# Kernel optimization log

Hardware: AMD Instinct MI355X
Metric: run time of the kernel (lower is better)

## Reference

```python
import jax, jax.numpy as jnp
import numpy as np

N, E, IN, HID, H, C, NL, OUT = 50000, 500000, 384, 128, 8, 16, 3, 16
NEG_SLOPE = 0.2

def setup_inputs() -> dict:
    key = jax.random.key(0)
    ks = jax.random.split(key, 16)
    s = 0.1
    return {
        "x": jax.random.normal(ks[0], (N, IN), jnp.float32),
        "edge_index": jax.random.randint(ks[1], (2, E), 0, N, jnp.int32),
        "proj_w": jax.random.normal(ks[2], (IN, HID), jnp.float32) * s,
        "proj_b": jax.random.normal(ks[3], (HID,), jnp.float32) * s,
        "lin_w": jax.random.normal(ks[4], (NL, HID, HID), jnp.float32) * s,
        "att_src": jax.random.normal(ks[5], (NL, H, C), jnp.float32) * s,
        "att_dst": jax.random.normal(ks[6], (NL, H, C), jnp.float32) * s,
        "gat_b": jax.random.normal(ks[7], (NL, HID), jnp.float32) * s,
        "ln_g": jnp.ones((NL, HID), jnp.float32),
        "ln_b": jnp.zeros((NL, HID), jnp.float32),
        "cls_w1": jax.random.normal(ks[8], (HID, HID // 2), jnp.float32) * s,
        "cls_b1": jax.random.normal(ks[9], (HID // 2,), jnp.float32) * s,
        "cls_w2": jax.random.normal(ks[10], (HID // 2, OUT), jnp.float32) * s,
        "cls_b2": jax.random.normal(ks[11], (OUT,), jnp.float32) * s,
    }

def _layernorm(h, g, b, eps=1e-5):
    mu = jnp.mean(h, axis=-1, keepdims=True)
    var = jnp.var(h, axis=-1, keepdims=True)
    return (h - mu) * jax.lax.rsqrt(var + eps) * g + b

def _gat_layer(h, src, dst, w, a_src, a_dst, bias):
    # h: [N, HID]; per-head transform -> [N, H, C]
    xh = (h @ w).reshape(N, H, C)
    al_s = jnp.einsum('nhc,hc->nh', xh, a_src)   # [N, H]
    al_d = jnp.einsum('nhc,hc->nh', xh, a_dst)
    e = jax.nn.leaky_relu(al_s[src] + al_d[dst], NEG_SLOPE)  # [E+N, H]
    # segment softmax over incoming edges of each dst node
    m = jax.ops.segment_max(e, dst, num_segments=N)
    e = jnp.exp(e - m[dst])
    denom = jax.ops.segment_sum(e, dst, num_segments=N)
    alpha = e / (denom[dst] + 1e-16)
    msg = xh[src] * alpha[:, :, None]            # [E+N, H, C]
    out = jax.ops.segment_sum(msg, dst, num_segments=N)
    return out.reshape(N, H * C) + bias

def reference(x, edge_index, proj_w, proj_b, lin_w, att_src, att_dst, gat_b,
              ln_g, ln_b, cls_w1, cls_b1, cls_w2, cls_b2):
    loops = jnp.arange(N, dtype=edge_index.dtype)  # PyG GATConv adds self-loops
    src = jnp.concatenate([edge_index[0], loops])
    dst = jnp.concatenate([edge_index[1], loops])
    h = jax.nn.relu(x @ proj_w + proj_b)
    for l in range(NL):
        h_res = h
        h = _gat_layer(h, src, dst, lin_w[l], att_src[l], att_dst[l], gat_b[l])
        h = h + h_res
        h = jax.nn.relu(_layernorm(h, ln_g[l], ln_b[l]))
    logits = jax.nn.relu(h @ cls_w1 + cls_b1) @ cls_w2 + cls_b2
    return jax.nn.log_softmax(logits, axis=1)
```

## Files before the change

kernel.cpp:

```cpp
#include <hip/hip_runtime.h>
#include <hip/hip_bf16.h>
#include <math.h>

#define NN 50000
#define EE 500000
#define DIN 384
#define HIDD 128
#define NHEAD 8
#define OUTD 16

typedef __attribute__((ext_vector_type(8))) __bf16 bf16x8;
typedef __attribute__((ext_vector_type(4))) float f32x4;

__device__ __forceinline__ ushort f2bf(float f) {
  union { float f; unsigned u; } v; v.f = f;
  unsigned r = v.u + 0x7fffu + ((v.u >> 16) & 1u);
  return (ushort)(r >> 16);
}
__device__ __forceinline__ float bflo(unsigned w) {
  union { unsigned u; float f; } v; v.u = w << 16; return v.f;
}
__device__ __forceinline__ float bfhi(unsigned w) {
  union { unsigned u; float f; } v; v.u = w & 0xffff0000u; return v.f;
}

__global__ void zero_ints(int* p, int n) {
  int i = blockIdx.x * blockDim.x + threadIdx.x;
  if (i < n) p[i] = 0;
}

__global__ void hist_kernel(const int* __restrict__ dst, int* __restrict__ counts, int e) {
  int i = blockIdx.x * blockDim.x + threadIdx.x;
  if (i < e) atomicAdd(&counts[dst[i]], 1);
}

#define SCAN_BS 256
#define SCAN_NBLK ((NN + SCAN_BS - 1) / SCAN_BS)

__global__ __launch_bounds__(256) void partial_sums(const int* __restrict__ counts,
                                                    int* __restrict__ bsum, int n) {
  __shared__ int red[256];
  int i = blockIdx.x * 256 + threadIdx.x;
  red[threadIdx.x] = (i < n) ? counts[i] : 0;
  __syncthreads();
  #pragma unroll
  for (int off = 128; off; off >>= 1) {
    if (threadIdx.x < off) red[threadIdx.x] += red[threadIdx.x + off];
    __syncthreads();
  }
  if (threadIdx.x == 0) bsum[blockIdx.x] = red[0];
}

__global__ __launch_bounds__(256) void scan_bsums(const int* __restrict__ bsum,
                                                  int* __restrict__ boff, int nb) {
  __shared__ int buf[256];
  int t = threadIdx.x;
  int v = (t < nb) ? bsum[t] : 0;
  buf[t] = v;
  __syncthreads();
  #pragma unroll
  for (int off = 1; off < 256; off <<= 1) {
    int u = (t >= off) ? buf[t - off] : 0;
    __syncthreads();
    buf[t] += u;
    __syncthreads();
  }
  if (t < nb) boff[t] = buf[t] - v;
}

__global__ __launch_bounds__(256) void final_scan(const int* __restrict__ counts,
                                                  const int* __restrict__ boff,
                                                  int* __restrict__ rowptr,
                                                  int* __restrict__ woff, int n) {
  __shared__ int buf[256];
  int i = blockIdx.x * 256 + threadIdx.x;
  int t = threadIdx.x;
  int v = (i < n) ? counts[i] : 0;
  buf[t] = v;
  __syncthreads();
  #pragma unroll
  for (int off = 1; off < 256; off <<= 1) {
    int u = (t >= off) ? buf[t - off] : 0;
    __syncthreads();
    buf[t] += u;
    __syncthreads();
  }
  int excl = boff[blockIdx.x] + buf[t] - v;
  if (i < n) { rowptr[i] = excl; woff[i] = excl; }
  if (i == n - 1) rowptr[n] = excl + v;
}

__global__ void scatter_kernel(const int* __restrict__ src, const int* __restrict__ dst,
                               int* __restrict__ woff, int* __restrict__ col, int e) {
  int i = blockIdx.x * blockDim.x + threadIdx.x;
  if (i < e) {
    int p = atomicAdd(&woff[dst[i]], 1);
    col[p] = src[i];
  }
}

__global__ void prep_weights(const float* __restrict__ proj_w,
                             const float* __restrict__ lin_w,
                             const float* __restrict__ cls_w1,
                             const float* __restrict__ cls_w2,
                             ushort* __restrict__ wt) {
  int i = blockIdx.x * blockDim.x + threadIdx.x;
  if (i < 49152) {
    int k = i >> 7, n = i & 127;
    wt[n * 384 + k] = f2bf(proj_w[i]);
  } else if (i < 98304) {
    int j = i - 49152;
    int l = j >> 14, rem = j & 16383;
    int k = rem >> 7, n = rem & 127;
    wt[49152 + l * 16384 + n * 128 + k] = f2bf(lin_w[j]);
  } else if (i < 106496) {
    int j = i - 98304;
    int n = j >> 7, k = j & 127;
    wt[98304 + n * 128 + k] = f2bf(cls_w1[k * 64 + n]);
  } else if (i < 107520) {
    int j = i - 106496;
    int n = j >> 6, k = j & 63;
    wt[106496 + n * 64 + k] = f2bf(cls_w2[k * 16 + n]);
  }
}

#define LDS_STRIDE 72
template<typename AT, bool RELU_BIAS>
__global__ __launch_bounds__(256) void mfma_gemm64(const AT* __restrict__ A,
                                                   const ushort* __restrict__ Bt,
                                                   const float* __restrict__ bias,
                                                   ushort* __restrict__ C, int M, int K) {
  __shared__ ushort sA[64 * LDS_STRIDE];
  __shared__ ushort sB[128 * LDS_STRIDE];
  const int tid = threadIdx.x;
  const int wave = tid >> 6, lane = tid & 63;
  const int q = lane >> 4, lm = lane & 15;
  const int wr = wave >> 1, wc = wave & 1;
  const int m0 = blockIdx.x * 64;

  f32x4 acc[2][4];
  #pragma unroll
  for (int i = 0; i < 2; i++)
    #pragma unroll
    for (int j = 0; j < 4; j++) acc[i][j] = {0.f, 0.f, 0.f, 0.f};

  for (int k0 = 0; k0 < K; k0 += 64) {
    __syncthreads();
    if constexpr (sizeof(AT) == 4) {
      #pragma unroll
      for (int p = 0; p < 4; ++p) {
        int idx = p * 256 + tid;
        int r = idx >> 4;
        int c = (idx & 15) << 2;
        int row = min(m0 + r, M - 1);
        float4 v = *(const float4*)((const float*)A + (size_t)row * K + k0 + c);
        ushort4 u;
        u.x = f2bf(v.x); u.y = f2bf(v.y); u.z = f2bf(v.z); u.w = f2bf(v.w);
        *(ushort4*)&sA[r * LDS_STRIDE + c] = u;
      }
    } else {
      #pragma unroll
      for (int p = 0; p < 2; ++p) {
        int idx = p * 256 + tid;
        int r = idx >> 3;
        int c = (idx & 7) << 3;
        int row = min(m0 + r, M - 1);
        *(bf16x8*)&sA[r * LDS_STRIDE + c] =
            *(const bf16x8*)((const ushort*)A + (size_t)row * K + k0 + c);
      }
    }
    #pragma unroll
    for (int p = 0; p < 4; ++p) {
      int idx = p * 256 + tid;
      int r = idx >> 3;
      int c = (idx & 7) << 3;
      *(bf16x8*)&sB[r * LDS_STRIDE + c] = *(const bf16x8*)(Bt + (size_t)r * K + k0 + c);
    }
    __syncthreads();
    #pragma unroll
    for (int ks = 0; ks < 2; ++ks) {
      bf16x8 af[2], bfv[4];
      #pragma unroll
      for (int t = 0; t < 2; ++t)
        af[t] = *(const bf16x8*)&sA[(wr * 32 + t * 16 + lm) * LDS_STRIDE + ks * 32 + q * 8];
      #pragma unroll
      for (int t = 0; t < 4; ++t)
        bfv[t] = *(const bf16x8*)&sB[(wc * 64 + t * 16 + lm) * LDS_STRIDE + ks * 32 + q * 8];
      #pragma unroll
      for (int i = 0; i < 2; ++i)
        #pragma unroll
        for (int j = 0; j < 4; ++j)
          acc[i][j] = __builtin_amdgcn_mfma_f32_16x16x32_bf16(af[i], bfv[j], acc[i][j], 0, 0, 0);
    }
  }
  #pragma unroll
  for (int i = 0; i < 2; ++i) {
    #pragma unroll
    for (int r = 0; r < 4; ++r) {
      int row = m0 + wr * 32 + i * 16 + q * 4 + r;
      if (row < M) {
        #pragma unroll
        for (int j = 0; j < 4; ++j) {
          int colc = wc * 64 + j * 16 + lm;
          float v = acc[i][j][r];
          if (RELU_BIAS) { v += bias[colc]; v = fmaxf(v, 0.f); }
          C[(size_t)row * 128 + colc] = f2bf(v);
        }
      }
    }
  }
}

__global__ void att_logits_kernel(const ushort* __restrict__ xh,
                                  const float* __restrict__ att_s,
                                  const float* __restrict__ att_d,
                                  float* __restrict__ al_s, float* __restrict__ al_d, int n) {
  int t = blockIdx.x * blockDim.x + threadIdx.x;
  if (t >= n * NHEAD) return;
  int head = t & 7;
  const unsigned* xw = (const unsigned*)(xh + (size_t)t * 16);
  const float* as = att_s + head * 16;
  const float* ad = att_d + head * 16;
  float ss = 0.f, dd = 0.f;
  #pragma unroll
  for (int i = 0; i < 8; ++i) {
    unsigned w = xw[i];
    float x0 = bflo(w), x1 = bfhi(w);
    ss = fmaf(x0, as[i * 2], fmaf(x1, as[i * 2 + 1], ss));
    dd = fmaf(x0, ad[i * 2], fmaf(x1, ad[i * 2 + 1], dd));
  }
  al_s[t] = ss;
  al_d[t] = dd;
}

__global__ __launch_bounds__(256) void gat_aggregate(
    const ushort* __restrict__ xh, const float* __restrict__ al_s,
    const float* __restrict__ al_d, const int* __restrict__ rowptr,
    const int* __restrict__ col, const ushort* __restrict__ h_res,
    const float* __restrict__ gb, const float* __restrict__ lng,
    const float* __restrict__ lnb, ushort* __restrict__ h_out, int n) {
  const int lane = threadIdx.x & 63;
  const int node = (blockIdx.x * blockDim.x + threadIdx.x) >> 6;
  if (node >= n) return;
  const int e8 = lane >> 3;
  const int hh = lane & 7;
  const int head = lane >> 3;
  const unsigned* xw_base = (const unsigned*)xh;

  const int start = rowptr[node], end = rowptr[node + 1];
  const int T = end - start + 1;
  const float ald_c = al_d[node * 8 + hh];

  float m = -INFINITY, denom = 0.f, acc0 = 0.f, acc1 = 0.f;

  for (int c = 0; c < T; c += 8) {
    int it = c + e8;
    bool valid = it < T;
    int idx = start + it;
    int s = (valid && idx < end) ? col[idx] : node;
    float e = al_s[s * 8 + hh] + ald_c;
    e = (e > 0.f) ? e : 0.2f * e;
    if (!valid) e = -INFINITY;
    float cm = e;
    cm = fmaxf(cm, __shfl_xor(cm, 8));
    cm = fmaxf(cm, __shfl_xor(cm, 16));
    cm = fmaxf(cm, __shfl_xor(cm, 32));
    float newm = fmaxf(m, __shfl(cm, head));
    float newm_c = __shfl(newm, hh * 8);
    float p_lane = __expf(e - newm_c);
    float scale = __expf(m - newm);
    m = newm;
    unsigned xg[8];
    int sj[8];
    #pragma unroll
    for (int j = 0; j < 8; ++j) sj[j] = __shfl(s, j * 8);
    #pragma unroll
    for (int j = 0; j < 8; ++j) xg[j] = xw_base[(size_t)sj[j] * 64 + lane];
    denom *= scale; acc0 *= scale; acc1 *= scale;
    #pragma unroll
    for (int j = 0; j < 8; ++j) {
      float pj = __shfl(p_lane, j * 8 + head);
      denom += pj;
      acc0 = fmaf(pj, bflo(xg[j]), acc0);
      acc1 = fmaf(pj, bfhi(xg[j]), acc1);
    }
  }

  float inv = 1.f / denom;
  int c0 = lane * 2, c1 = c0 + 1;
  unsigned ur = ((const unsigned*)h_res)[(size_t)node * 64 + lane];
  float v0 = acc0 * inv + gb[c0] + bflo(ur);
  float v1 = acc1 * inv + gb[c1] + bfhi(ur);
  float sum = v0 + v1;
  #pragma unroll
  for (int off = 32; off; off >>= 1) sum += __shfl_xor(sum, off);
  float mean = sum * (1.f / 128.f);
  float d0 = v0 - mean, d1 = v1 - mean;
  float sq = d0 * d0 + d1 * d1;
  #pragma unroll
  for (int off = 32; off; off >>= 1) sq += __shfl_xor(sq, off);
  float rstd = rsqrtf(sq * (1.f / 128.f) + 1e-5f);
  float o0 = fmaxf(d0 * rstd * lng[c0] + lnb[c0], 0.f);
  float o1 = fmaxf(d1 * rstd * lng[c1] + lnb[c1], 0.f);
  ((unsigned*)h_out)[(size_t)node * 64 + lane] =
      (unsigned)f2bf(o0) | ((unsigned)f2bf(o1) << 16);
}

#define CSTR 136
#define HSTR 72
__global__ __launch_bounds__(256) void classifier_mfma(
    const ushort* __restrict__ h, const ushort* __restrict__ w1t,
    const float* __restrict__ b1, const ushort* __restrict__ w2t,
    const float* __restrict__ b2, float* __restrict__ out, int n) {
  __shared__ ushort sA[128 * CSTR];
  __shared__ ushort sB[64 * CSTR];
  __shared__ ushort sHid[128 * HSTR];
  const int tid = threadIdx.x;
  const int wave = tid >> 6, lane = tid & 63;
  const int q = lane >> 4, lm = lane & 15;
  const int wr = wave >> 1, wc = wave & 1;
  const int m0 = blockIdx.x * 128;

  #pragma unroll
  for (int p = 0; p < 8; ++p) {
    int idx = p * 256 + tid;
    int r = idx >> 4;
    int c = (idx & 15) << 3;
    int row = min(m0 + r, n - 1);
    *(bf16x8*)&sA[r * CSTR + c] = *(const bf16x8*)(h + (size_t)row * 128 + c);
  }
  #pragma unroll
  for (int p = 0; p < 4; ++p) {
    int idx = p * 256 + tid;
    int r = idx >> 4;
    int c = (idx & 15) << 3;
    *(bf16x8*)&sB[r * CSTR + c] = *(const bf16x8*)(w1t + r * 128 + c);
  }
  __syncthreads();

  f32x4 acc[4][2];
  #pragma unroll
  for (int i = 0; i < 4; ++i)
    #pragma unroll
    for (int j = 0; j < 2; ++j) acc[i][j] = {0.f, 0.f, 0.f, 0.f};
  #pragma unroll
  for (int ks = 0; ks < 4; ++ks) {
    bf16x8 af[4], bfv[2];
    #pragma unroll
    for (int t = 0; t < 4; ++t)
      af[t] = *(const bf16x8*)&sA[(wr * 64 + t * 16 + lm) * CSTR + ks * 32 + q * 8];
    #pragma unroll
    for (int j = 0; j < 2; ++j)
      bfv[j] = *(const bf16x8*)&sB[(wc * 32 + j * 16 + lm) * CSTR + ks * 32 + q * 8];
    #pragma unroll
    for (int i = 0; i < 4; ++i)
      #pragma unroll
      for (int j = 0; j < 2; ++j)
        acc[i][j] = __builtin_amdgcn_mfma_f32_16x16x32_bf16(af[i], bfv[j], acc[i][j], 0, 0, 0);
  }
  #pragma unroll
  for (int i = 0; i < 4; ++i) {
    #pragma unroll
    for (int j = 0; j < 2; ++j) {
      int colc = wc * 32 + j * 16 + lm;
      float bb = b1[colc];
      #pragma unroll
      for (int r = 0; r < 4; ++r) {
        int row = wr * 64 + i * 16 + q * 4 + r;
        float v = fmaxf(acc[i][j][r] + bb, 0.f);
        sHid[row * HSTR + colc] = f2bf(v);
      }
    }
  }
  __syncthreads();

  f32x4 acc2[2] = {{0.f, 0.f, 0.f, 0.f}, {0.f, 0.f, 0.f, 0.f}};
  #pragma unroll
  for (int ks = 0; ks < 2; ++ks) {
    bf16x8 b2f = *(const bf16x8*)(w2t + lm * 64 + ks * 32 + q * 8);
    #pragma unroll
    for (int t = 0; t < 2; ++t) {
      bf16x8 a2 = *(const bf16x8*)&sHid[(wave * 32 + t * 16 + lm) * HSTR + ks * 32 + q * 8];
      acc2[t] = __builtin_amdgcn_mfma_f32_16x16x32_bf16(a2, b2f, acc2[t], 0, 0, 0);
    }
  }
  float bb2 = b2[lm];
  #pragma unroll
  for (int t = 0; t < 2; ++t) {
    #pragma unroll
    for (int r = 0; r < 4; ++r) {
      int row = m0 + wave * 32 + t * 16 + q * 4 + r;
      float lg = acc2[t][r] + bb2;
      float mx = lg;
      #pragma unroll
      for (int off = 8; off; off >>= 1) mx = fmaxf(mx, __shfl_xor(mx, off, 16));
      float se = __expf(lg - mx);
      #pragma unroll
      for (int off = 8; off; off >>= 1) se += __shfl_xor(se, off, 16);
      if (row < n) out[(size_t)row * 16 + lm] = lg - mx - __logf(se);
    }
  }
}

extern "C" void kernel_launch(void* const* d_in, const int* in_sizes, int n_in,
                              void* d_out, int out_size, void* d_ws, size_t ws_size,
                              hipStream_t stream) {
  const float* x       = (const float*)d_in[0];
  const int*   ei      = (const int*)d_in[1];
  const float* proj_w  = (const float*)d_in[2];
  const float* proj_b  = (const float*)d_in[3];
  const float* lin_w   = (const float*)d_in[4];
  const float* att_src = (const float*)d_in[5];
  const float* att_dst = (const float*)d_in[6];
  const float* gat_b   = (const float*)d_in[7];
  const float* ln_g    = (const float*)d_in[8];
  const float* ln_b    = (const float*)d_in[9];
  const float* cls_w1  = (const float*)d_in[10];
  const float* cls_b1  = (const float*)d_in[11];
  const float* cls_w2  = (const float*)d_in[12];
  const float* cls_b2  = (const float*)d_in[13];
  float* outp = (float*)d_out;

  const int N = NN, E = EE;
  ushort* wt   = (ushort*)d_ws;
  ushort* h0   = wt + 108544;
  ushort* h1   = h0 + (size_t)N * 128;
  ushort* xh_u = h1 + (size_t)N * 128;
  float* als   = (float*)(xh_u + (size_t)N * 128);
  float* ald   = als + (size_t)N * NHEAD;
  int* counts  = (int*)(ald + (size_t)N * NHEAD);
  int* rowptr  = counts + N;
  int* woff    = rowptr + N + 1;
  int* col     = woff + N;
  int* bsum    = col + E;
  int* boff    = bsum + SCAN_NBLK;

  const int* e_src = ei;
  const int* e_dst = ei + E;

  prep_weights<<<(107520 + 255) / 256, 256, 0, stream>>>(proj_w, lin_w, cls_w1, cls_w2, wt);

  zero_ints<<<(N + 255) / 256, 256, 0, stream>>>(counts, N);
  hist_kernel<<<(E + 255) / 256, 256, 0, stream>>>(e_dst, counts, E);
  partial_sums<<<SCAN_NBLK, 256, 0, stream>>>(counts, bsum, N);
  scan_bsums<<<1, 256, 0, stream>>>(bsum, boff, SCAN_NBLK);
  final_scan<<<SCAN_NBLK, 256, 0, stream>>>(counts, boff, rowptr, woff, N);
  scatter_kernel<<<(E + 255) / 256, 256, 0, stream>>>(e_src, e_dst, woff, col, E);

  const int gblocks = (N + 63) / 64;
  mfma_gemm64<float, true><<<gblocks, 256, 0, stream>>>(x, wt, proj_b, h0, N, DIN);

  ushort* hc = h0;
  ushort* hn = h1;
  for (int l = 0; l < 3; ++l) {
    mfma_gemm64<ushort, false><<<gblocks, 256, 0, stream>>>(
        hc, wt + 49152 + l * 16384, nullptr, xh_u, N, 128);
    att_logits_kernel<<<(N * NHEAD + 255) / 256, 256, 0, stream>>>(
        xh_u, att_src + l * 128, att_dst + l * 128, als, ald, N);
    gat_aggregate<<<(N + 3) / 4, 256, 0, stream>>>(
        xh_u, als, ald, rowptr, col, hc, gat_b + l * 128, ln_g + l * 128,
        ln_b + l * 128, hn, N);
    ushort* t = hc; hc = hn; hn = t;
  }
  classifier_mfma<<<(N + 127) / 128, 256, 0, stream>>>(
      hc, wt + 98304, cls_b1, wt + 106496, cls_b2, outp, N);
}
```

Measured before the change: 380.2 us.

## Fuse attention logits into GAT GEMM epilogue and widen aggregate gather batch

Removes the separate attention-logit kernel by computing the per-head src/dst dot products in the GEMM epilogue, reducing across the 16 columns of each head with lane shuffles on the fp32 accumulators. This saves a kernel launch and a re-read of xh per layer. The aggregate kernel now processes 16 edges per iteration, issuing two batches of neighbour-row gathers before the softmax math to keep more loads in flight. In exchange, logits now come from fp32 accumulators rather than bf16-rounded values, the epilogue carries many extra shuffles, and the wider loop adds per-edge branches and register pressure.

```diff
diff --git a/kernel.cpp b/kernel.cpp
--- a/kernel.cpp
+++ b/kernel.cpp
@@ -125,11 +125,16 @@
 }
 
 #define LDS_STRIDE 72
-template<typename AT, bool RELU_BIAS>
+template<typename AT, bool RELU_BIAS, bool ATT>
 __global__ __launch_bounds__(256) void mfma_gemm64(const AT* __restrict__ A,
                                                    const ushort* __restrict__ Bt,
                                                    const float* __restrict__ bias,
-                                                   ushort* __restrict__ C, int M, int K) {
+                                                   ushort* __restrict__ C,
+                                                   const float* __restrict__ att_s,
+                                                   const float* __restrict__ att_d,
+                                                   float* __restrict__ al_s,
+                                                   float* __restrict__ al_d,
+                                                   int M, int K) {
   __shared__ ushort sA[64 * LDS_STRIDE];
   __shared__ ushort sB[128 * LDS_STRIDE];
   const int tid = threadIdx.x;
@@ -191,6 +196,14 @@
         #pragma unroll
         for (int j = 0; j < 4; ++j)
           acc[i][j] = __builtin_amdgcn_mfma_f32_16x16x32_bf16(af[i], bfv[j], acc[i][j], 0, 0, 0);
+    }
+  }
+  float asw[4], adw[4];
+  if constexpr (ATT) {
+    #pragma unroll
+    for (int j = 0; j < 4; ++j) {
+      asw[j] = att_s[(wc * 4 + j) * 16 + lm];
+      adw[j] = att_d[(wc * 4 + j) * 16 + lm];
     }
   }
   #pragma unroll
@@ -209,28 +222,31 @@
       }
     }
   }
-}
-
-__global__ void att_logits_kernel(const ushort* __restrict__ xh,
-                                  const float* __restrict__ att_s,
-                                  const float* __restrict__ att_d,
-                                  float* __restrict__ al_s, float* __restrict__ al_d, int n) {
-  int t = blockIdx.x * blockDim.x + threadIdx.x;
-  if (t >= n * NHEAD) return;
-  int head = t & 7;
-  const unsigned* xw = (const unsigned*)(xh + (size_t)t * 16);
-  const float* as = att_s + head * 16;
-  const float* ad = att_d + head * 16;
-  float ss = 0.f, dd = 0.f;
-  #pragma unroll
-  for (int i = 0; i < 8; ++i) {
-    unsigned w = xw[i];
-    float x0 = bflo(w), x1 = bfhi(w);
-    ss = fmaf(x0, as[i * 2], fmaf(x1, as[i * 2 + 1], ss));
-    dd = fmaf(x0, ad[i * 2], fmaf(x1, ad[i * 2 + 1], dd));
-  }
-  al_s[t] = ss;
-  al_d[t] = dd;
+  if constexpr (ATT) {
+    #pragma unroll
+    for (int i = 0; i < 2; ++i) {
+      #pragma unroll
+      for (int j = 0; j < 4; ++j) {
+        #pragma unroll
+        for (int r = 0; r < 4; ++r) {
+          float ss = acc[i][j][r] * asw[j];
+          float dd = acc[i][j][r] * adw[j];
+          #pragma unroll
+          for (int off = 1; off < 16; off <<= 1) {
+            ss += __shfl_xor(ss, off);
+            dd += __shfl_xor(dd, off);
+          }
+          if (lm == 0) {
+            int row = m0 + wr * 32 + i * 16 + q * 4 + r;
+            if (row < M) {
+              al_s[row * 8 + wc * 4 + j] = ss;
+              al_d[row * 8 + wc * 4 + j] = dd;
+            }
+          }
+        }
+      }
+    }
+  }
 }
 
 __global__ __launch_bounds__(256) void gat_aggregate(
@@ -253,37 +269,61 @@
 
   float m = -INFINITY, denom = 0.f, acc0 = 0.f, acc1 = 0.f;
 
-  for (int c = 0; c < T; c += 8) {
-    int it = c + e8;
-    bool valid = it < T;
-    int idx = start + it;
-    int s = (valid && idx < end) ? col[idx] : node;
-    float e = al_s[s * 8 + hh] + ald_c;
-    e = (e > 0.f) ? e : 0.2f * e;
-    if (!valid) e = -INFINITY;
-    float cm = e;
+  for (int c = 0; c < T; c += 16) {
+    int it0 = c + e8, it1 = c + 8 + e8;
+    int idx0 = start + it0, idx1 = start + it1;
+    int s0 = (it0 < T && idx0 < end) ? col[idx0] : node;
+    int s1 = (it1 < T && idx1 < end) ? col[idx1] : node;
+
+    unsigned xg0[8], xg1[8];
+    #pragma unroll
+    for (int j = 0; j < 8; ++j)
+      if (c + j < T) {
+        int sj = __shfl(s0, j * 8);
+        xg0[j] = xw_base[(size_t)sj * 64 + lane];
+      }
+    #pragma unroll
+    for (int j = 0; j < 8; ++j)
+      if (c + 8 + j < T) {
+        int sj = __shfl(s1, j * 8);
+        xg1[j] = xw_base[(size_t)sj * 64 + lane];
+      }
+
+    float e0 = al_s[s0 * 8 + hh] + ald_c;
+    e0 = (e0 > 0.f) ? e0 : 0.2f * e0;
+    if (it0 >= T) e0 = -INFINITY;
+    float e1 = al_s[s1 * 8 + hh] + ald_c;
+    e1 = (e1 > 0.f) ? e1 : 0.2f * e1;
+    if (it1 >= T) e1 = -INFINITY;
+
+    float cm = fmaxf(e0, e1);
     cm = fmaxf(cm, __shfl_xor(cm, 8));
     cm = fmaxf(cm, __shfl_xor(cm, 16));
     cm = fmaxf(cm, __shfl_xor(cm, 32));
     float newm = fmaxf(m, __shfl(cm, head));
     float newm_c = __shfl(newm, hh * 8);
-    float p_lane = __expf(e - newm_c);
+    float p0 = __expf(e0 - newm_c);
+    float p1 = __expf(e1 - newm_c);
     float scale = __expf(m - newm);
     m = newm;
-    unsigned xg[8];
-    int sj[8];
-    #pragma unroll
-    for (int j = 0; j < 8; ++j) sj[j] = __shfl(s, j * 8);
-    #pragma unroll
-    for (int j = 0; j < 8; ++j) xg[j] = xw_base[(size_t)sj[j] * 64 + lane];
+
     denom *= scale; acc0 *= scale; acc1 *= scale;
     #pragma unroll
-    for (int j = 0; j < 8; ++j) {
-      float pj = __shfl(p_lane, j * 8 + head);
-      denom += pj;
-      acc0 = fmaf(pj, bflo(xg[j]), acc0);
-      acc1 = fmaf(pj, bfhi(xg[j]), acc1);
-    }
+    for (int j = 0; j < 8; ++j)
+      if (c + j < T) {
+        float pj = __shfl(p0, j * 8 + head);
+        denom += pj;
+        acc0 = fmaf(pj, bflo(xg0[j]), acc0);
+        acc1 = fmaf(pj, bfhi(xg0[j]), acc1);
+      }
+    #pragma unroll
+    for (int j = 0; j < 8; ++j)
+      if (c + 8 + j < T) {
+        float pj = __shfl(p1, j * 8 + head);
+        denom += pj;
+        acc0 = fmaf(pj, bflo(xg1[j]), acc0);
+        acc1 = fmaf(pj, bfhi(xg1[j]), acc1);
+      }
   }
 
   float inv = 1.f / denom;
@@ -448,15 +488,15 @@
   scatter_kernel<<<(E + 255) / 256, 256, 0, stream>>>(e_src, e_dst, woff, col, E);
 
   const int gblocks = (N + 63) / 64;
-  mfma_gemm64<float, true><<<gblocks, 256, 0, stream>>>(x, wt, proj_b, h0, N, DIN);
+  mfma_gemm64<float, true, false><<<gblocks, 256, 0, stream>>>(
+      x, wt, proj_b, h0, nullptr, nullptr, nullptr, nullptr, N, DIN);
 
   ushort* hc = h0;
   ushort* hn = h1;
   for (int l = 0; l < 3; ++l) {
-    mfma_gemm64<ushort, false><<<gblocks, 256, 0, stream>>>(
-        hc, wt + 49152 + l * 16384, nullptr, xh_u, N, 128);
-    att_logits_kernel<<<(N * NHEAD + 255) / 256, 256, 0, stream>>>(
-        xh_u, att_src + l * 128, att_dst + l * 128, als, ald, N);
+    mfma_gemm64<ushort, false, true><<<gblocks, 256, 0, stream>>>(
+        hc, wt + 49152 + l * 16384, nullptr, xh_u,
+        att_src + l * 128, att_dst + l * 128, als, ald, N, 128);
     gat_aggregate<<<(N + 3) / 4, 256, 0, stream>>>(
         xh_u, als, ald, rowptr, col, hc, gat_b + l * 128, ln_g + l * 128,
         ln_b + l * 128, hn, N);
```

Result: slower. 402.5 us (+5.9%).

## Fuse attention logits into GEMM epilogue and shrink GEMM tile to 32 rows

Applied to the files above, without the earlier changes.

Computes the per-head attention logits in the layer GEMM epilogue using shuffle reductions over the fp32 accumulators, which removes the separate att_logits kernel and its re-read of xh. The GEMM tile drops from 64 to 32 rows, giving twice as many blocks for occupancy, and K becomes a template constant. The trade-off is that each block now re-reads the full B matrix for half as many rows, and the logits come from fp32 accumulators instead of bf16-rounded values.

```diff
diff --git a/kernel.cpp b/kernel.cpp
--- a/kernel.cpp
+++ b/kernel.cpp
@@ -125,83 +125,93 @@
 }
 
 #define LDS_STRIDE 72
-template<typename AT, bool RELU_BIAS>
-__global__ __launch_bounds__(256) void mfma_gemm64(const AT* __restrict__ A,
+template<typename AT, int KK, bool RELU_BIAS, bool ATT>
+__global__ __launch_bounds__(256) void mfma_gemm32(const AT* __restrict__ A,
                                                    const ushort* __restrict__ Bt,
                                                    const float* __restrict__ bias,
-                                                   ushort* __restrict__ C, int M, int K) {
-  __shared__ ushort sA[64 * LDS_STRIDE];
+                                                   ushort* __restrict__ C,
+                                                   const float* __restrict__ att_s,
+                                                   const float* __restrict__ att_d,
+                                                   float* __restrict__ al_s,
+                                                   float* __restrict__ al_d,
+                                                   int M) {
+  constexpr bool F32A = (sizeof(AT) == 4);
+  __shared__ ushort sA[32 * LDS_STRIDE];
   __shared__ ushort sB[128 * LDS_STRIDE];
   const int tid = threadIdx.x;
-  const int wave = tid >> 6, lane = tid & 63;
+  const int w = tid >> 6, lane = tid & 63;
   const int q = lane >> 4, lm = lane & 15;
-  const int wr = wave >> 1, wc = wave & 1;
-  const int m0 = blockIdx.x * 64;
-
-  f32x4 acc[2][4];
+  const int m0 = blockIdx.x * 32;
+
+  f32x4 acc[2][2];
   #pragma unroll
   for (int i = 0; i < 2; i++)
     #pragma unroll
-    for (int j = 0; j < 4; j++) acc[i][j] = {0.f, 0.f, 0.f, 0.f};
-
-  for (int k0 = 0; k0 < K; k0 += 64) {
-    __syncthreads();
-    if constexpr (sizeof(AT) == 4) {
-      #pragma unroll
-      for (int p = 0; p < 4; ++p) {
+    for (int j = 0; j < 2; j++) acc[i][j] = {0.f, 0.f, 0.f, 0.f};
+
+  for (int k0 = 0; k0 < KK; k0 += 64) {
+    __syncthreads();
+    if constexpr (F32A) {
+      #pragma unroll
+      for (int p = 0; p < 2; ++p) {
         int idx = p * 256 + tid;
         int r = idx >> 4;
         int c = (idx & 15) << 2;
         int row = min(m0 + r, M - 1);
-        float4 v = *(const float4*)((const float*)A + (size_t)row * K + k0 + c);
+        float4 v = *(const float4*)((const float*)A + (size_t)row * KK + k0 + c);
         ushort4 u;
         u.x = f2bf(v.x); u.y = f2bf(v.y); u.z = f2bf(v.z); u.w = f2bf(v.w);
         *(ushort4*)&sA[r * LDS_STRIDE + c] = u;
       }
     } else {
-      #pragma unroll
-      for (int p = 0; p < 2; ++p) {
-        int idx = p * 256 + tid;
-        int r = idx >> 3;
-        int c = (idx & 7) << 3;
-        int row = min(m0 + r, M - 1);
-        *(bf16x8*)&sA[r * LDS_STRIDE + c] =
-            *(const bf16x8*)((const ushort*)A + (size_t)row * K + k0 + c);
-      }
+      int r = tid >> 3;
+      int c = (tid & 7) << 3;
+      int row = min(m0 + r, M - 1);
+      *(bf16x8*)&sA[r * LDS_STRIDE + c] =
+          *(const bf16x8*)((const ushort*)A + (size_t)row * KK + k0 + c);
     }
     #pragma unroll
     for (int p = 0; p < 4; ++p) {
       int idx = p * 256 + tid;
       int r = idx >> 3;
       int c = (idx & 7) << 3;
-      *(bf16x8*)&sB[r * LDS_STRIDE + c] = *(const bf16x8*)(Bt + (size_t)r * K + k0 + c);
+      *(bf16x8*)&sB[r * LDS_STRIDE + c] = *(const bf16x8*)(Bt + (size_t)r * KK + k0 + c);
     }
     __syncthreads();
     #pragma unroll
     for (int ks = 0; ks < 2; ++ks) {
-      bf16x8 af[2], bfv[4];
-      #pragma unroll
-      for (int t = 0; t < 2; ++t)
-        af[t] = *(const bf16x8*)&sA[(wr * 32 + t * 16 + lm) * LDS_STRIDE + ks * 32 + q * 8];
-      #pragma unroll
-      for (int t = 0; t < 4; ++t)
-        bfv[t] = *(const bf16x8*)&sB[(wc * 64 + t * 16 + lm) * LDS_STRIDE + ks * 32 + q * 8];
+      bf16x8 af[2], bfv[2];
+      #pragma unroll
+      for (int i = 0; i < 2; ++i)
+        af[i] = *(const bf16x8*)&sA[(i * 16 + lm) * LDS_STRIDE + ks * 32 + q * 8];
+      #pragma unroll
+      for (int j = 0; j < 2; ++j)
+        bfv[j] = *(const bf16x8*)&sB[(w * 32 + j * 16 + lm) * LDS_STRIDE + ks * 32 + q * 8];
       #pragma unroll
       for (int i = 0; i < 2; ++i)
         #pragma unroll
-        for (int j = 0; j < 4; ++j)
+        for (int j = 0; j < 2; ++j)
           acc[i][j] = __builtin_amdgcn_mfma_f32_16x16x32_bf16(af[i], bfv[j], acc[i][j], 0, 0, 0);
     }
   }
+
+  float asw[2], adw[2];
+  if constexpr (ATT) {
+    #pragma unroll
+    for (int j = 0; j < 2; ++j) {
+      asw[j] = att_s[(w * 2 + j) * 16 + lm];
+      adw[j] = att_d[(w * 2 + j) * 16 + lm];
+    }
+  }
   #pragma unroll
   for (int i = 0; i < 2; ++i) {
     #pragma unroll
     for (int r = 0; r < 4; ++r) {
-      int row = m0 + wr * 32 + i * 16 + q * 4 + r;
+      int row = m0 + i * 16 + q * 4 + r;
       if (row < M) {
         #pragma unroll
-        for (int j = 0; j < 4; ++j) {
-          int colc = wc * 64 + j * 16 + lm;
+        for (int j = 0; j < 2; ++j) {
+          int colc = w * 32 + j * 16 + lm;
           float v = acc[i][j][r];
           if (RELU_BIAS) { v += bias[colc]; v = fmaxf(v, 0.f); }
           C[(size_t)row * 128 + colc] = f2bf(v);
@@ -209,28 +219,31 @@
       }
     }
   }
-}
-
-__global__ void att_logits_kernel(const ushort* __restrict__ xh,
-                                  const float* __restrict__ att_s,
-                                  const float* __restrict__ att_d,
-                                  float* __restrict__ al_s, float* __restrict__ al_d, int n) {
-  int t = blockIdx.x * blockDim.x + threadIdx.x;
-  if (t >= n * NHEAD) return;
-  int head = t & 7;
-  const unsigned* xw = (const unsigned*)(xh + (size_t)t * 16);
-  const float* as = att_s + head * 16;
-  const float* ad = att_d + head * 16;
-  float ss = 0.f, dd = 0.f;
-  #pragma unroll
-  for (int i = 0; i < 8; ++i) {
-    unsigned w = xw[i];
-    float x0 = bflo(w), x1 = bfhi(w);
-    ss = fmaf(x0, as[i * 2], fmaf(x1, as[i * 2 + 1], ss));
-    dd = fmaf(x0, ad[i * 2], fmaf(x1, ad[i * 2 + 1], dd));
-  }
-  al_s[t] = ss;
-  al_d[t] = dd;
+  if constexpr (ATT) {
+    #pragma unroll
+    for (int i = 0; i < 2; ++i) {
+      #pragma unroll
+      for (int j = 0; j < 2; ++j) {
+        #pragma unroll
+        for (int r = 0; r < 4; ++r) {
+          float ss = acc[i][j][r] * asw[j];
+          float dd = acc[i][j][r] * adw[j];
+          #pragma unroll
+          for (int off = 1; off < 16; off <<= 1) {
+            ss += __shfl_xor(ss, off);
+            dd += __shfl_xor(dd, off);
+          }
+          if (lm == 0) {
+            int row = m0 + i * 16 + q * 4 + r;
+            if (row < M) {
+              al_s[row * 8 + w * 2 + j] = ss;
+              al_d[row * 8 + w * 2 + j] = dd;
+            }
+          }
+        }
+      }
+    }
+  }
 }
 
 __global__ __launch_bounds__(256) void gat_aggregate(
@@ -447,16 +460,16 @@
   final_scan<<<SCAN_NBLK, 256, 0, stream>>>(counts, boff, rowptr, woff, N);
   scatter_kernel<<<(E + 255) / 256, 256, 0, stream>>>(e_src, e_dst, woff, col, E);
 
-  const int gblocks = (N + 63) / 64;
-  mfma_gemm64<float, true><<<gblocks, 256, 0, stream>>>(x, wt, proj_b, h0, N, DIN);
+  const int gblocks = (N + 31) / 32;
+  mfma_gemm32<float, DIN, true, false><<<gblocks, 256, 0, stream>>>(
+      x, wt, proj_b, h0, nullptr, nullptr, nullptr, nullptr, N);
 
   ushort* hc = h0;
   ushort* hn = h1;
   for (int l = 0; l < 3; ++l) {
-    mfma_gemm64<ushort, false><<<gblocks, 256, 0, stream>>>(
-        hc, wt + 49152 + l * 16384, nullptr, xh_u, N, 128);
-    att_logits_kernel<<<(N * NHEAD + 255) / 256, 256, 0, stream>>>(
-        xh_u, att_src + l * 128, att_dst + l * 128, als, ald, N);
+    mfma_gemm32<ushort, HIDD, false, true><<<gblocks, 256, 0, stream>>>(
+        hc, wt + 49152 + l * 16384, nullptr, xh_u,
+        att_src + l * 128, att_dst + l * 128, als, ald, N);
     gat_aggregate<<<(N + 3) / 4, 256, 0, stream>>>(
         xh_u, als, ald, rowptr, col, hc, gat_b + l * 128, ln_g + l * 128,
         ln_b + l * 128, hn, N);
```

New measurement: 385.7 us. Within noise of the previous version (+1.4%).
